# Performance work log

Hardware: AMD Instinct MI355X
Metric: run time of the kernel (lower is better)

The kernel has to match this reference:

```python
import jax, jax.numpy as jnp
import numpy as np

ABITS = 4
WBITS = 4
BN_EPS = 1e-5


def _ste(x, q):
    # straight-through estimator: forward q, backward identity
    return x + jax.lax.stop_gradient(q - x)


def act_quant(x):
    # unsigned activation quantization to ABITS (clipped-ReLU style, as in NIPQ quantized act)
    levels = (1 << ABITS) - 1  # 15
    xc = jnp.clip(x, 0.0, 1.0)
    q = jnp.round(xc * levels) / levels
    return _ste(xc, q)


def weight_quant(w):
    # symmetric per-tensor weight quantization to WBITS
    n = (1 << (WBITS - 1)) - 1  # 7
    alpha = jnp.max(jnp.abs(w)) + 1e-12
    wc = jnp.clip(w / alpha, -1.0, 1.0)
    q = jnp.round(wc * n) / n * alpha
    return _ste(w, q)


def conv3x3(x, w):
    # NCHW, OIHW, stride 1, padding 1
    return jax.lax.conv_general_dilated(
        x, w, window_strides=(1, 1), padding=((1, 1), (1, 1)),
        dimension_numbers=('NCHW', 'OIHW', 'NCHW'))


def batchnorm(x, gamma, beta):
    # training-mode BN: batch statistics over (N,H,W)
    mean = jnp.mean(x, axis=(0, 2, 3), keepdims=True)
    var = jnp.var(x, axis=(0, 2, 3), keepdims=True)
    xhat = (x - mean) * jax.lax.rsqrt(var + BN_EPS)
    return xhat * gamma[None, :, None, None] + beta[None, :, None, None]


def setup_inputs() -> dict:
    key = jax.random.key(0)
    k = jax.random.split(key, 3)
    C = 128
    x = jax.random.normal(k[0], (64, C, 56, 56), dtype=jnp.float32)
    w1 = jax.random.normal(k[1], (C, C, 3, 3), dtype=jnp.float32) * 0.05
    w2 = jax.random.normal(k[2], (C, C, 3, 3), dtype=jnp.float32) * 0.05
    return {
        'x': x, 'w1': w1, 'w2': w2,
        'gamma1': jnp.ones((C,), jnp.float32), 'beta1': jnp.zeros((C,), jnp.float32),
        'gamma2': jnp.ones((C,), jnp.float32), 'beta2': jnp.zeros((C,), jnp.float32),
    }


def reference(x, w1, w2, gamma1, beta1, gamma2, beta2):
    identity = x
    out = act_quant(x)
    out = conv3x3(out, weight_quant(w1))
    out = batchnorm(out, gamma1, beta1)
    out = act_quant(out)
    out = conv3x3(out, weight_quant(w2))
    out = batchnorm(out, gamma2, beta2)
    return out + identity
```

## Files before the change

### kernel.cpp

```cpp
#include <hip/hip_runtime.h>

#define CH    128
#define IMG   56
#define PADW  58
#define HWSZ  3136
#define NPIX  200704
#define WELEMS 147456
#define BNEPS 1e-5f
#define PADB  430592
#define YOFF  27557888u
#define Y2OFF_B 51380224u
#define WQ1OFF_B 78938112u

typedef float f32x4 __attribute__((ext_vector_type(4)));
typedef short short8 __attribute__((ext_vector_type(8)));
typedef _Float16 f16;

__device__ __forceinline__ void async16(const void* g, void* l) {
  __builtin_amdgcn_global_load_lds(
      (const __attribute__((address_space(1))) unsigned int*)g,
      (__attribute__((address_space(3))) unsigned int*)l, 16, 0, 0);
}
__device__ __forceinline__ unsigned char fp8enc(float v) {
  return (unsigned char)(__builtin_amdgcn_cvt_pk_fp8_f32(v, v, 0, false) & 0xFF);
}
__device__ __forceinline__ void bn_inline(int lin, const float* stats, const unsigned* abits,
                                          const float* g, const float* b, float* bnpS) {
  if (lin < 128) {
    const float inv = 1.f / (float)NPIX;
    float gs   = (__uint_as_float(*abits) + 1e-12f) * (1.f / 105.f);
    float mean = stats[lin] * inv;
    float var  = fmaxf(stats[CH + lin] * inv - mean * mean, 0.f);
    float sc   = g[lin] * gs * rsqrtf(gs * gs * var + BNEPS);
    bnpS[lin]      = sc;
    bnpS[CH + lin] = b[lin] - sc * mean;
  }
}
__device__ __forceinline__ void halo_zero(unsigned char* qb, int lin) {
  for (int i = lin; i < 1824; i += 256) {
    size_t off;
    if (i < 464)      off = (size_t)i * 16;
    else if (i < 928) off = (size_t)57 * PADW * 128 + (size_t)(i - 464) * 16;
    else {
      int j = i - 928, loc = j >> 3, sub = j & 7;
      int row = 1 + (loc >> 1), col = (loc & 1) ? 57 : 0;
      off = ((size_t)row * PADW + col) * 128 + (size_t)sub * 16;
    }
    *(uint4*)(qb + off) = (uint4){0u, 0u, 0u, 0u};
  }
}

__global__ void k_wmax(const float* __restrict__ w1, const float* __restrict__ w2,
                       unsigned* __restrict__ alpha_bits) {
  int idx = blockIdx.x * 256 + threadIdx.x;
  float m1 = 0.f, m2 = 0.f;
  for (int i = idx; i < WELEMS; i += gridDim.x * 256) {
    m1 = fmaxf(m1, fabsf(w1[i]));
    m2 = fmaxf(m2, fabsf(w2[i]));
  }
#pragma unroll
  for (int off = 32; off > 0; off >>= 1) {
    m1 = fmaxf(m1, __shfl_xor(m1, off));
    m2 = fmaxf(m2, __shfl_xor(m2, off));
  }
  __shared__ float s1[4], s2[4];
  int wave = threadIdx.x >> 6;
  if ((threadIdx.x & 63) == 0) { s1[wave] = m1; s2[wave] = m2; }
  __syncthreads();
  if (threadIdx.x == 0) {
    m1 = fmaxf(fmaxf(s1[0], s1[1]), fmaxf(s1[2], s1[3]));
    m2 = fmaxf(fmaxf(s2[0], s2[1]), fmaxf(s2[2], s2[3]));
    atomicMax(&alpha_bits[0], __float_as_uint(m1));
    atomicMax(&alpha_bits[1], __float_as_uint(m2));
  }
}

__global__ void k_wquant(const float* __restrict__ w1, const float* __restrict__ w2,
                         const unsigned* __restrict__ alpha_bits,
                         unsigned char* __restrict__ wq1, unsigned char* __restrict__ wq2) {
  int idx = blockIdx.x * 256 + threadIdx.x;
  int t = idx >= WELEMS;
  int j = t ? idx - WELEMS : idx;
  int kk  = j >> 14;
  int rem = j & 16383;
  int co = rem >> 7, ci = rem & 127;
  float alpha = __uint_as_float(alpha_bits[t]) + 1e-12f;
  float v  = (t ? w2 : w1)[co * 1152 + ci * 9 + kk];
  float wc = fminf(fmaxf(v / alpha, -1.f), 1.f);
  (t ? wq2 : wq1)[j] = fp8enc(rintf(wc * 7.f));
}

__global__ void k_actq(const float* __restrict__ x, unsigned char* __restrict__ qx) {
  __shared__ float tile[32][33];
  int n = blockIdx.z, p0 = blockIdx.x * 32, c0 = blockIdx.y * 32;
  int tx = threadIdx.x, ty = threadIdx.y, lin = ty * 32 + tx;
  unsigned char* qb = qx + (size_t)n * PADB;
  if (blockIdx.x == 0 && blockIdx.y == 0) halo_zero(qb, lin);
  const float* xs = x + ((size_t)n * CH + c0) * HWSZ;
#pragma unroll
  for (int r = 0; r < 4; ++r) {
    int c = ty + r * 8;
    float v = xs[(size_t)c * HWSZ + p0 + tx];
    v = fminf(fmaxf(v, 0.f), 1.f);
    tile[c][tx] = rintf(v * 15.f);
  }
  __syncthreads();
#pragma unroll
  for (int r = 0; r < 4; ++r) {
    int pl = p0 + ty + r * 8;
    int h = pl / IMG, w = pl - h * IMG;
    qb[((h + 1) * PADW + (w + 1)) * 128 + c0 + tx] = fp8enc(tile[tx][ty + r * 8]);
  }
}

#define CONV_SETUP(PCALC)                                                        \
  const int tid  = threadIdx.x;                                                  \
  const int lane = tid & 63;                                                     \
  const int quad = lane >> 4, lrow = lane & 15;                                  \
  const int m_off = ((tid >> 6) >> 1) * 64, n_off = ((tid >> 6) & 1) * 64;       \
  char* As = smem; char* Bs = smem + 16384;                                      \
  const unsigned char* asrc[4]; int boff[4], ldsoff[4];                          \
  _Pragma("unroll")                                                              \
  for (int i = 0; i < 4; ++i) {                                                  \
    int c = i * 256 + tid;                                                       \
    int r = c >> 3;                                                              \
    int srccol = ((c & 7) ^ (r & 7)) * 16;          \
    ldsoff[i] = (i * 256 + (tid & ~63)) * 16;                                    \
    PCALC                                                                        \
    boff[i] = r * 128 + srccol;                                                  \
  }                                                                              \
  int axcol[4];                                                                  \
  _Pragma("unroll")                                                              \
  for (int ks = 0; ks < 4; ++ks)                                                 \
    axcol[ks] = ((((ks << 1) | (quad >> 1)) ^ (lrow & 7)) << 4) | ((quad & 1) << 3); \
  f32x4 acc[4][4];                                                               \
  _Pragma("unroll")                                                              \
  for (int mi = 0; mi < 4; ++mi)                                                 \
    _Pragma("unroll")                                                            \
    for (int ni = 0; ni < 4; ++ni) acc[mi][ni] = (f32x4){0.f, 0.f, 0.f, 0.f};

#define PCALC_GLOBAL                                                             \
    int p = blockIdx.x * 128 + r;                                                \
    int n = p / HWSZ, l = p - n * HWSZ;                                          \
    int h = l / IMG, w = l - h * IMG;                                            \
    asrc[i] = act + (size_t)n * PADB + ((h + 1) * PADW + (w + 1)) * 128 + srccol;

#define PCALC_IMG                                                                \
    int p = blockIdx.x * 128 + r;                                                \
    if (p > HWSZ - 1) p = HWSZ - 1;              \
    int h = p / IMG, w = p - h * IMG;                                            \
    asrc[i] = act + ((h + 1) * PADW + (w + 1)) * 128 + srccol;

#define CONV_KLOOP(WQ)                                                           \
  for (int kk = 0; kk < 9; ++kk) {                                               \
    const int doff = ((kk / 3 - 1) * PADW + (kk % 3 - 1)) * 128;                 \
    __syncthreads();                                                             \
    _Pragma("unroll")                                                            \
    for (int i = 0; i < 4; ++i) async16(asrc[i] + doff, As + ldsoff[i]);         \
    _Pragma("unroll")                                                            \
    for (int i = 0; i < 4; ++i) async16((WQ) + kk * 16384 + boff[i], Bs + ldsoff[i]); \
    __syncthreads();                                                             \
    _Pragma("unroll")                                                            \
    for (int ks = 0; ks < 4; ++ks) {                                             \
      long af[4], bf[4];                                                         \
      _Pragma("unroll")                                                          \
      for (int mi = 0; mi < 4; ++mi)                                             \
        af[mi] = *(const long*)(As + (m_off + mi * 16 + lrow) * 128 + axcol[ks]); \
      _Pragma("unroll")                                                          \
      for (int ni = 0; ni < 4; ++ni)                                             \
        bf[ni] = *(const long*)(Bs + (n_off + ni * 16 + lrow) * 128 + axcol[ks]); \
      _Pragma("unroll")                                                          \
      for (int mi = 0; mi < 4; ++mi)                                             \
        _Pragma("unroll")                                                        \
        for (int ni = 0; ni < 4; ++ni)                                           \
          acc[mi][ni] = __builtin_amdgcn_mfma_f32_16x16x32_fp8_fp8(af[mi], bf[ni], acc[mi][ni], 0, 0, 0); \
    }                                                                            \
  }

__global__ __launch_bounds__(256, 3)
void k_conv(const unsigned char* __restrict__ act, const unsigned char* __restrict__ wq,
            short* __restrict__ y, float* __restrict__ stats) {
  __shared__ __align__(16) char smem[33792];
  CONV_SETUP(PCALC_GLOBAL)
  CONV_KLOOP(wq)
  float lsum[4] = {0.f, 0.f, 0.f, 0.f}, lsq[4] = {0.f, 0.f, 0.f, 0.f};
#pragma unroll
  for (int mi = 0; mi < 4; ++mi) {
    int prow = blockIdx.x * 128 + m_off + mi * 16 + quad * 4;
#pragma unroll
    for (int ni = 0; ni < 4; ++ni) {
      int co = n_off + ni * 16 + lrow;
#pragma unroll
      for (int rg = 0; rg < 4; ++rg) {
        float v = acc[mi][ni][rg];
        y[(size_t)(prow + rg) * CH + co] = (short)fminf(fmaxf(v, -32767.f), 32767.f);
        lsum[ni] += v; lsq[ni] += v * v;
      }
    }
  }
#pragma unroll
  for (int ni = 0; ni < 4; ++ni) {
    lsum[ni] += __shfl_xor(lsum[ni], 16); lsum[ni] += __shfl_xor(lsum[ni], 32);
    lsq[ni]  += __shfl_xor(lsq[ni], 16);  lsq[ni]  += __shfl_xor(lsq[ni], 32);
  }
  __syncthreads();
  float* red = (float*)(smem + 32768);
  red[tid] = 0.f;
  __syncthreads();
  if (quad == 0) {
#pragma unroll
    for (int ni = 0; ni < 4; ++ni) {
      int co = n_off + ni * 16 + lrow;
      atomicAdd(&red[co], lsum[ni]);
      atomicAdd(&red[CH + co], lsq[ni]);
    }
  }
  __syncthreads();
  atomicAdd(&stats[tid], red[tid]);
}

__global__ void k_bnq(const short* __restrict__ y, const float* __restrict__ stats,
                      const unsigned* __restrict__ abits, const float* __restrict__ g,
                      const float* __restrict__ b, unsigned char* __restrict__ q) {
  __shared__ float bnpS[256];
  int tid = threadIdx.x;
  bn_inline(tid, stats, abits, g, b, bnpS);
  if (blockIdx.x < 64) halo_zero(q + (size_t)blockIdx.x * PADB, tid);
  __syncthreads();
  size_t i = (size_t)blockIdx.x * 256 + tid;
  short8 v = ((const short8*)y)[i];
  int c0 = (int)((i * 8) & (CH - 1));
  int pix = (int)(i >> 4);
  int n = pix / HWSZ, l = pix - n * HWSZ;
  int h = l / IMG, w = l - h * IMG;
  float t[8];
#pragma unroll
  for (int j = 0; j < 8; ++j) {
    float u = (float)v[j] * bnpS[c0 + j] + bnpS[CH + c0 + j];
    t[j] = rintf(fminf(fmaxf(u, 0.f), 1.f) * 15.f);
  }
  int lo = __builtin_amdgcn_cvt_pk_fp8_f32(t[0], t[1], 0, false);
  lo     = __builtin_amdgcn_cvt_pk_fp8_f32(t[2], t[3], lo, true);
  int hi = __builtin_amdgcn_cvt_pk_fp8_f32(t[4], t[5], 0, false);
  hi     = __builtin_amdgcn_cvt_pk_fp8_f32(t[6], t[7], hi, true);
  *(uint2*)(q + (size_t)n * PADB + ((h + 1) * PADW + (w + 1)) * 128 + c0) =
      (uint2){(unsigned)lo, (unsigned)hi};
}

__global__ void k_fin(const short* __restrict__ y2, const float* __restrict__ stats,
                      const unsigned* __restrict__ abits, const float* __restrict__ g,
                      const float* __restrict__ b, const float* __restrict__ x,
                      float* __restrict__ out, int img0) {
  __shared__ float bnpS[256];
  __shared__ float tile[32][33];
  int tx = threadIdx.x, ty = threadIdx.y, lin = ty * 32 + tx;
  bn_inline(lin, stats, abits, g, b, bnpS);
  __syncthreads();
  int n = img0 + blockIdx.z, p0 = blockIdx.x * 32, c0 = blockIdx.y * 32;
  const short* ys = y2 + (size_t)n * HWSZ * CH;
  float sc = bnpS[c0 + tx], sh = bnpS[CH + c0 + tx];
#pragma unroll
  for (int r = 0; r < 4; ++r) {
    int p = p0 + ty + r * 8;
    tile[ty + r * 8][tx] = (float)ys[(size_t)p * CH + c0 + tx] * sc + sh;
  }
  __syncthreads();
  const float* xs = x + ((size_t)n * CH + c0) * HWSZ;
  float*       os = out + ((size_t)n * CH + c0) * HWSZ;
#pragma unroll
  for (int r = 0; r < 4; ++r) {
    int c = ty + r * 8;
    size_t a = (size_t)c * HWSZ + p0 + tx;
    os[a] = tile[tx][c] + xs[a];
  }
}

__global__ __launch_bounds__(256, 3)
void k_conv_out63(const unsigned char* __restrict__ act, const unsigned char* __restrict__ wq,
                  const float* __restrict__ stats, const unsigned* __restrict__ abits,
                  const float* __restrict__ g, const float* __restrict__ b,
                  const float* __restrict__ x, float* __restrict__ out) {
  __shared__ __align__(16) char smem[33792];
  __shared__ float bnpS[256];
  bn_inline(threadIdx.x, stats, abits, g, b, bnpS);
  CONV_SETUP(PCALC_IMG)
  CONV_KLOOP(wq)
  __syncthreads();
  f16 (*tile)[132] = (f16(*)[132])smem;
#pragma unroll
  for (int ni = 0; ni < 4; ++ni) {
    int co = n_off + ni * 16 + lrow;
    float sc = bnpS[co], sh = bnpS[CH + co];
#pragma unroll
    for (int mi = 0; mi < 4; ++mi) {
      int pr = m_off + mi * 16 + quad * 4;
#pragma unroll
      for (int rg = 0; rg < 4; ++rg)
        tile[co][pr + rg] = (f16)(acc[mi][ni][rg] * sc + sh);
    }
  }
  __syncthreads();
  int c = tid >> 1, seg = tid & 1;
  int pl0 = blockIdx.x * 128 + seg * 64;
  if (pl0 < HWSZ) {
    size_t gb = ((size_t)63 * CH + c) * HWSZ + pl0;
    const float* xp = x + gb;
    float* op = out + gb;
    const f16* tr = &tile[c][seg * 64];
#pragma unroll
    for (int j = 0; j < 64; j += 4) {
      f32x4 xv = *(const f32x4*)(xp + j);
      f32x4 ov;
      ov[0] = (float)tr[j]     + xv[0];
      ov[1] = (float)tr[j + 1] + xv[1];
      ov[2] = (float)tr[j + 2] + xv[2];
      ov[3] = (float)tr[j + 3] + xv[3];
      *(f32x4*)(op + j) = ov;
    }
  }
}

extern "C" void kernel_launch(void* const* d_in, const int* in_sizes, int n_in,
                              void* d_out, int out_size, void* d_ws, size_t ws_size,
                              hipStream_t stream) {
  (void)in_sizes; (void)n_in; (void)out_size;
  const float* x  = (const float*)d_in[0];
  const float* w1 = (const float*)d_in[1];
  const float* w2 = (const float*)d_in[2];
  const float* g1 = (const float*)d_in[3];
  const float* b1 = (const float*)d_in[4];
  const float* g2 = (const float*)d_in[5];
  const float* b2 = (const float*)d_in[6];
  float* out = (float*)d_out;

  char* dob = (char*)d_out;
  unsigned char* q1p = (unsigned char*)dob;
  unsigned char* q2p = (unsigned char*)dob;
  short* y1 = (short*)(dob + YOFF);

  char* ws = (char*)d_ws;
  unsigned* alpha_bits = (unsigned*)ws;
  float* stats1 = (float*)(ws + 256);
  float* stats2 = (float*)(ws + 1280);

  const bool bigws = ws_size >= 51679744u;
  unsigned char *wq1, *wq2;
  short* y2;
  if (bigws) {
    wq1 = (unsigned char*)(ws + 4608);
    wq2 = (unsigned char*)(ws + 152064);
    y2  = (short*)(ws + 299520);
  } else {
    wq1 = (unsigned char*)(dob + WQ1OFF_B);
    wq2 = (unsigned char*)(ws + 4608);
    y2  = (short*)(dob + Y2OFF_B);
  }
  unsigned char* q63p = (unsigned char*)(ws + 152064);

  hipMemsetAsync(ws, 0, 4608, stream);
  k_wmax  <<<64, 256, 0, stream>>>(w1, w2, alpha_bits);
  k_wquant<<<2 * WELEMS / 256, 256, 0, stream>>>(w1, w2, alpha_bits, wq1, wq2);
  k_actq  <<<dim3(98, 4, 64), dim3(32, 8), 0, stream>>>(x, q1p);
  k_conv  <<<NPIX / 128, 256, 0, stream>>>(q1p, wq1, y1, stats1);
  k_bnq   <<<NPIX * CH / 2048, 256, 0, stream>>>(y1, stats1, alpha_bits + 0, g1, b1, q2p);
  k_conv  <<<NPIX / 128, 256, 0, stream>>>(q2p, wq2, y2, stats2);

  if (bigws) {
    k_fin <<<dim3(98, 4, 64), dim3(32, 8), 0, stream>>>(y2, stats2, alpha_bits + 1, g2, b2, x, out, 0);
  } else {
    hipMemcpyAsync(q63p, q2p + (size_t)63 * PADB, PADB, hipMemcpyDeviceToDevice, stream);
    k_fin <<<dim3(98, 4, 32), dim3(32, 8), 0, stream>>>(y2, stats2, alpha_bits + 1, g2, b2, x, out, 0);
    k_fin <<<dim3(98, 4, 16), dim3(32, 8), 0, stream>>>(y2, stats2, alpha_bits + 1, g2, b2, x, out, 32);
    k_fin <<<dim3(98, 4,  8), dim3(32, 8), 0, stream>>>(y2, stats2, alpha_bits + 1, g2, b2, x, out, 48);
    k_fin <<<dim3(98, 4,  4), dim3(32, 8), 0, stream>>>(y2, stats2, alpha_bits + 1, g2, b2, x, out, 56);
    k_fin <<<dim3(98, 4,  2), dim3(32, 8), 0, stream>>>(y2, stats2, alpha_bits + 1, g2, b2, x, out, 60);
    k_fin <<<dim3(98, 4,  1), dim3(32, 8), 0, stream>>>(y2, stats2, alpha_bits + 1, g2, b2, x, out, 62);
    k_conv_out63<<<25, 256, 0, stream>>>(q63p, wq2, stats2, alpha_bits + 1, g2, b2, x, out);
  }
}
```

Measured before the change: 381.3 us.

## Switch conv GEMMs to int8 MFMA and double-buffer LDS tiles

Quantized activations and weights are stored as plain int8 integers instead of fp8 encodings, and the conv inner loop now uses the 16x16x64 i8 MFMA with 16-byte fragment loads and int32 accumulators. The K loop is restructured to double-buffer the A/B tiles in LDS, prefetching the next tap while computing the current one, with one barrier per iteration and raised wave priority around the MFMAs. LDS per block doubles and launch bounds drop from 3 to 2 blocks per CU, which trades occupancy for overlap and a higher-throughput int8 instruction.

Measured after the change: 370.5 us. 2.8% less time.

```diff
diff --git a/kernel.cpp b/kernel.cpp
--- a/kernel.cpp
+++ b/kernel.cpp
@@ -13,6 +13,7 @@
 #define WQ1OFF_B 78938112u
 
 typedef float f32x4 __attribute__((ext_vector_type(4)));
+typedef int   i32x4 __attribute__((ext_vector_type(4)));
 typedef short short8 __attribute__((ext_vector_type(8)));
 typedef _Float16 f16;
 
@@ -20,9 +21,6 @@
   __builtin_amdgcn_global_load_lds(
       (const __attribute__((address_space(1))) unsigned int*)g,
       (__attribute__((address_space(3))) unsigned int*)l, 16, 0, 0);
-}
-__device__ __forceinline__ unsigned char fp8enc(float v) {
-  return (unsigned char)(__builtin_amdgcn_cvt_pk_fp8_f32(v, v, 0, false) & 0xFF);
 }
 __device__ __forceinline__ void bn_inline(int lin, const float* stats, const unsigned* abits,
                                           const float* g, const float* b, float* bnpS) {
@@ -87,7 +85,8 @@
   float alpha = __uint_as_float(alpha_bits[t]) + 1e-12f;
   float v  = (t ? w2 : w1)[co * 1152 + ci * 9 + kk];
   float wc = fminf(fmaxf(v / alpha, -1.f), 1.f);
-  (t ? wq2 : wq1)[j] = fp8enc(rintf(wc * 7.f));
+  int q = (int)rintf(wc * 7.f);
+  (t ? wq2 : wq1)[j] = (unsigned char)(q & 0xFF);
 }
 
 __global__ void k_actq(const float* __restrict__ x, unsigned char* __restrict__ qx) {
@@ -109,7 +108,7 @@
   for (int r = 0; r < 4; ++r) {
     int pl = p0 + ty + r * 8;
     int h = pl / IMG, w = pl - h * IMG;
-    qb[((h + 1) * PADW + (w + 1)) * 128 + c0 + tx] = fp8enc(tile[tx][ty + r * 8]);
+    qb[((h + 1) * PADW + (w + 1)) * 128 + c0 + tx] = (unsigned char)(int)tile[tx][ty + r * 8];
   }
 }
 
@@ -118,7 +117,6 @@
   const int lane = tid & 63;                                                     \
   const int quad = lane >> 4, lrow = lane & 15;                                  \
   const int m_off = ((tid >> 6) >> 1) * 64, n_off = ((tid >> 6) & 1) * 64;       \
-  char* As = smem; char* Bs = smem + 16384;                                      \
   const unsigned char* asrc[4]; int boff[4], ldsoff[4];                          \
   _Pragma("unroll")                                                              \
   for (int i = 0; i < 4; ++i) {                                                  \
@@ -129,15 +127,15 @@
     PCALC                                                                        \
     boff[i] = r * 128 + srccol;                                                  \
   }                                                                              \
-  int axcol[4];                                                                  \
+  int acol[2];                                                                   \
   _Pragma("unroll")                                                              \
-  for (int ks = 0; ks < 4; ++ks)                                                 \
-    axcol[ks] = ((((ks << 1) | (quad >> 1)) ^ (lrow & 7)) << 4) | ((quad & 1) << 3); \
-  f32x4 acc[4][4];                                                               \
+  for (int j = 0; j < 2; ++j)                                                    \
+    acol[j] = ((4 * j + quad) ^ (lrow & 7)) << 4;                                \
+  i32x4 acc[4][4];                                                               \
   _Pragma("unroll")                                                              \
   for (int mi = 0; mi < 4; ++mi)                                                 \
     _Pragma("unroll")                                                            \
-    for (int ni = 0; ni < 4; ++ni) acc[mi][ni] = (f32x4){0.f, 0.f, 0.f, 0.f};
+    for (int ni = 0; ni < 4; ++ni) acc[mi][ni] = (i32x4){0, 0, 0, 0};
 
 #define PCALC_GLOBAL                                                             \
     int p = blockIdx.x * 128 + r;                                                \
@@ -152,35 +150,49 @@
     asrc[i] = act + ((h + 1) * PADW + (w + 1)) * 128 + srccol;
 
 #define CONV_KLOOP(WQ)                                                           \
+  {                 \
+    _Pragma("unroll")                                                            \
+    for (int i = 0; i < 4; ++i) async16(asrc[i] - (PADW + 1) * 128, smem + ldsoff[i]); \
+    _Pragma("unroll")                                                            \
+    for (int i = 0; i < 4; ++i) async16((WQ) + boff[i], smem + 16384 + ldsoff[i]); \
+    __syncthreads();                                                             \
+  }                                                                              \
   for (int kk = 0; kk < 9; ++kk) {                                               \
-    const int doff = ((kk / 3 - 1) * PADW + (kk % 3 - 1)) * 128;                 \
-    __syncthreads();                                                             \
+    if (kk < 8) {                      \
+      const int kn = kk + 1;                                                     \
+      const int doff = ((kn / 3 - 1) * PADW + (kn % 3 - 1)) * 128;               \
+      char* nb = smem + ((kn & 1) << 15);                                        \
+      _Pragma("unroll")                                                          \
+      for (int i = 0; i < 4; ++i) async16(asrc[i] + doff, nb + ldsoff[i]);       \
+      _Pragma("unroll")                                                          \
+      for (int i = 0; i < 4; ++i) async16((WQ) + kn * 16384 + boff[i], nb + 16384 + ldsoff[i]); \
+    }                                                                            \
+    const char* As = smem + ((kk & 1) << 15);                                    \
+    const char* Bs = As + 16384;                                                 \
+    __builtin_amdgcn_s_setprio(1);                                               \
     _Pragma("unroll")                                                            \
-    for (int i = 0; i < 4; ++i) async16(asrc[i] + doff, As + ldsoff[i]);         \
-    _Pragma("unroll")                                                            \
-    for (int i = 0; i < 4; ++i) async16((WQ) + kk * 16384 + boff[i], Bs + ldsoff[i]); \
-    __syncthreads();                                                             \
-    _Pragma("unroll")                                                            \
-    for (int ks = 0; ks < 4; ++ks) {                                             \
-      long af[4], bf[4];                                                         \
+    for (int j = 0; j < 2; ++j) {                                                \
+      i32x4 af[4], bf[4];                                                        \
       _Pragma("unroll")                                                          \
       for (int mi = 0; mi < 4; ++mi)                                             \
-        af[mi] = *(const long*)(As + (m_off + mi * 16 + lrow) * 128 + axcol[ks]); \
+        af[mi] = *(const i32x4*)(As + (m_off + mi * 16 + lrow) * 128 + acol[j]); \
       _Pragma("unroll")                                                          \
       for (int ni = 0; ni < 4; ++ni)                                             \
-        bf[ni] = *(const long*)(Bs + (n_off + ni * 16 + lrow) * 128 + axcol[ks]); \
+        bf[ni] = *(const i32x4*)(Bs + (n_off + ni * 16 + lrow) * 128 + acol[j]); \
       _Pragma("unroll")                                                          \
       for (int mi = 0; mi < 4; ++mi)                                             \
         _Pragma("unroll")                                                        \
         for (int ni = 0; ni < 4; ++ni)                                           \
-          acc[mi][ni] = __builtin_amdgcn_mfma_f32_16x16x32_fp8_fp8(af[mi], bf[ni], acc[mi][ni], 0, 0, 0); \
+          acc[mi][ni] = __builtin_amdgcn_mfma_i32_16x16x64_i8(af[mi], bf[ni], acc[mi][ni], 0, 0, 0); \
     }                                                                            \
-  }
-
-__global__ __launch_bounds__(256, 3)
+    __builtin_amdgcn_s_setprio(0);                                               \
+    __syncthreads();     \
+  }
+
+__global__ __launch_bounds__(256, 2)
 void k_conv(const unsigned char* __restrict__ act, const unsigned char* __restrict__ wq,
             short* __restrict__ y, float* __restrict__ stats) {
-  __shared__ __align__(16) char smem[33792];
+  __shared__ __align__(16) char smem[66560];
   CONV_SETUP(PCALC_GLOBAL)
   CONV_KLOOP(wq)
   float lsum[4] = {0.f, 0.f, 0.f, 0.f}, lsq[4] = {0.f, 0.f, 0.f, 0.f};
@@ -192,7 +204,7 @@
       int co = n_off + ni * 16 + lrow;
 #pragma unroll
       for (int rg = 0; rg < 4; ++rg) {
-        float v = acc[mi][ni][rg];
+        float v = (float)acc[mi][ni][rg];
         y[(size_t)(prow + rg) * CH + co] = (short)fminf(fmaxf(v, -32767.f), 32767.f);
         lsum[ni] += v; lsq[ni] += v * v;
       }
@@ -204,7 +216,7 @@
     lsq[ni]  += __shfl_xor(lsq[ni], 16);  lsq[ni]  += __shfl_xor(lsq[ni], 32);
   }
   __syncthreads();
-  float* red = (float*)(smem + 32768);
+  float* red = (float*)(smem + 65536);
   red[tid] = 0.f;
   __syncthreads();
   if (quad == 0) {
@@ -233,18 +245,15 @@
   int pix = (int)(i >> 4);
   int n = pix / HWSZ, l = pix - n * HWSZ;
   int h = l / IMG, w = l - h * IMG;
-  float t[8];
+  unsigned lo = 0u, hi = 0u;
 #pragma unroll
   for (int j = 0; j < 8; ++j) {
     float u = (float)v[j] * bnpS[c0 + j] + bnpS[CH + c0 + j];
-    t[j] = rintf(fminf(fmaxf(u, 0.f), 1.f) * 15.f);
-  }
-  int lo = __builtin_amdgcn_cvt_pk_fp8_f32(t[0], t[1], 0, false);
-  lo     = __builtin_amdgcn_cvt_pk_fp8_f32(t[2], t[3], lo, true);
-  int hi = __builtin_amdgcn_cvt_pk_fp8_f32(t[4], t[5], 0, false);
-  hi     = __builtin_amdgcn_cvt_pk_fp8_f32(t[6], t[7], hi, true);
+    unsigned qv = (unsigned)(int)rintf(fminf(fmaxf(u, 0.f), 1.f) * 15.f);
+    if (j < 4) lo |= qv << (8 * j); else hi |= qv << (8 * (j - 4));
+  }
   *(uint2*)(q + (size_t)n * PADB + ((h + 1) * PADW + (w + 1)) * 128 + c0) =
-      (uint2){(unsigned)lo, (unsigned)hi};
+      (uint2){lo, hi};
 }
 
 __global__ void k_fin(const short* __restrict__ y2, const float* __restrict__ stats,
@@ -275,12 +284,12 @@
   }
 }
 
-__global__ __launch_bounds__(256, 3)
+__global__ __launch_bounds__(256, 2)
 void k_conv_out63(const unsigned char* __restrict__ act, const unsigned char* __restrict__ wq,
                   const float* __restrict__ stats, const unsigned* __restrict__ abits,
                   const float* __restrict__ g, const float* __restrict__ b,
                   const float* __restrict__ x, float* __restrict__ out) {
-  __shared__ __align__(16) char smem[33792];
+  __shared__ __align__(16) char smem[66560];
   __shared__ float bnpS[256];
   bn_inline(threadIdx.x, stats, abits, g, b, bnpS);
   CONV_SETUP(PCALC_IMG)
@@ -296,7 +305,7 @@
       int pr = m_off + mi * 16 + quad * 4;
 #pragma unroll
       for (int rg = 0; rg < 4; ++rg)
-        tile[co][pr + rg] = (f16)(acc[mi][ni][rg] * sc + sh);
+        tile[co][pr + rg] = (f16)((float)acc[mi][ni][rg] * sc + sh);
     }
   }
   __syncthreads();
```
